# Kernel tuning notes

Measured on AMD Instinct MI355X. Metric: run time of the kernel, lower is better.

The kernel has to match this reference:

```python
import jax, jax.numpy as jnp
import numpy as np

N_NODES = 10000
N_EDGES = 160000
F_IN = 128
H = 8          # heads (both layers)
C1 = 64        # conv1 per-head channels
C2 = 64        # conv2 per-head channels (= out_channels)
NEG_SLOPE = 0.2
EPS = 1e-16


def setup_inputs() -> dict:
    key = jax.random.key(0)
    ks = jax.random.split(key, 12)
    x = jax.random.normal(ks[0], (N_NODES, F_IN), dtype=jnp.float32)
    edge_index = jax.random.randint(ks[1], (2, N_EDGES), 0, N_NODES, dtype=jnp.int32)
    s = lambda fan: float(1.0 / np.sqrt(fan))
    # conv1 params
    W1 = jax.random.normal(ks[2], (F_IN, H * C1), dtype=jnp.float32) * s(F_IN)
    att_src1 = jax.random.normal(ks[3], (H, C1), dtype=jnp.float32) * s(C1)
    att_dst1 = jax.random.normal(ks[4], (H, C1), dtype=jnp.float32) * s(C1)
    bias1 = jnp.zeros((H * C1,), dtype=jnp.float32)
    t1 = jnp.ones((), dtype=jnp.float32)  # SoftmaxAggregation learnable temperature
    # conv2 params (input = H*C1 = 512)
    W2 = jax.random.normal(ks[5], (H * C1, H * C2), dtype=jnp.float32) * s(H * C1)
    att_src2 = jax.random.normal(ks[6], (H, C2), dtype=jnp.float32) * s(C2)
    att_dst2 = jax.random.normal(ks[7], (H, C2), dtype=jnp.float32) * s(C2)
    bias2 = jnp.zeros((H * C2,), dtype=jnp.float32)
    t2 = jnp.ones((), dtype=jnp.float32)
    return {"x": x, "edge_index": edge_index,
            "W1": W1, "att_src1": att_src1, "att_dst1": att_dst1, "bias1": bias1, "t1": t1,
            "W2": W2, "att_src2": att_src2, "att_dst2": att_dst2, "bias2": bias2, "t2": t2}


def _seg_softmax_weights(logits, seg, n):
    # numerically stable softmax over segments (per trailing dims)
    mx = jax.ops.segment_max(logits, seg, num_segments=n)
    mx = jnp.where(jnp.isfinite(mx), mx, 0.0)  # empty segments -> 0
    ex = jnp.exp(logits - mx[seg])
    den = jax.ops.segment_sum(ex, seg, num_segments=n)
    return ex / (den[seg] + EPS)


def gat_layer(x, src, dst, W, a_src, a_dst, bias, t, n):
    # GATConv (add_self_loops=False, concat=True) with SoftmaxAggregation(learn=True)
    h = (x @ W).reshape(n, *a_src.shape)                      # [N,H,C]
    alpha_s = jnp.sum(h * a_src, axis=-1)                     # [N,H]
    alpha_d = jnp.sum(h * a_dst, axis=-1)                     # [N,H]
    e = jax.nn.leaky_relu(alpha_s[src] + alpha_d[dst], NEG_SLOPE)  # [E,H]
    alpha = _seg_softmax_weights(e, dst, n)                   # attention softmax per dst
    m = h[src] * alpha[:, :, None]                            # [E,H,C] messages
    w = _seg_softmax_weights(t * m, dst, n)                   # learnable softmax aggregation
    out = jax.ops.segment_sum(w * m, dst, num_segments=n)     # [N,H,C]
    return out.reshape(n, -1) + bias


def reference(x, edge_index, W1, att_src1, att_dst1, bias1, t1,
              W2, att_src2, att_dst2, bias2, t2):
    src, dst = edge_index[0], edge_index[1]
    n = x.shape[0]
    h = jax.nn.relu(gat_layer(x, src, dst, W1, att_src1, att_dst1, bias1, t1, n))
    return jax.nn.relu(gat_layer(h, src, dst, W2, att_src2, att_dst2, bias2, t2, n))
```

## Files before the change

### kernel.cpp

```cpp
#include <hip/hip_runtime.h>
#include <hip/hip_bf16.h>

#define NN 10000
#define NE 160000
#define NH 8
#define NC 64
#define NF 512
#define NEG_SLOPE 0.2f
#define SEPS 1e-16f
#define L2E 1.44269504f

typedef __attribute__((ext_vector_type(8))) short s8v;
typedef __attribute__((ext_vector_type(4))) float f4v;

__device__ __forceinline__ float lrelu(float x) { return x > 0.f ? x : NEG_SLOPE * x; }

__device__ __forceinline__ unsigned short bf16_rn(float f) {
  unsigned int u = __float_as_uint(f);
  return (unsigned short)((u + 0x7FFFu + ((u >> 16) & 1u)) >> 16);
}
__device__ __forceinline__ float bf16_to_f32(unsigned short h) {
  return __uint_as_float(((unsigned int)h) << 16);
}

__global__ void zero_kernel(int* __restrict__ p, int n) {
  int i = blockIdx.x * blockDim.x + threadIdx.x;
  if (i < n) p[i] = 0;
}

__global__ void hist_kernel(const int* __restrict__ dst, int* __restrict__ counts) {
  int e = blockIdx.x * blockDim.x + threadIdx.x;
  if (e < NE) atomicAdd(&counts[dst[e]], 1);
}

__global__ __launch_bounds__(1024) void scan_fast(const int* __restrict__ counts,
                                                  int* __restrict__ row_ptr) {
  __shared__ int part[1024];
  const int tid = threadIdx.x;
  const int base = tid * 16;
  int loc[16];
  int s = 0;
#pragma unroll
  for (int i = 0; i < 16; ++i) {
    int idx = base + i;
    int v = (idx < NN) ? counts[idx] : 0;
    loc[i] = s;
    s += v;
  }
  part[tid] = s;
  __syncthreads();
  for (int off = 1; off < 1024; off <<= 1) {
    int t = (tid >= off) ? part[tid - off] : 0;
    __syncthreads();
    part[tid] += t;
    __syncthreads();
  }
  int pre = (tid > 0) ? part[tid - 1] : 0;
#pragma unroll
  for (int i = 0; i < 16; ++i) {
    int idx = base + i;
    if (idx < NN) row_ptr[idx] = pre + loc[i];
  }
  if (tid == 1023) row_ptr[NN] = part[1023];
}

__global__ void scatter_kernel(const int* __restrict__ dst, const int* __restrict__ row_ptr,
                               int* __restrict__ cursor, int* __restrict__ sorted) {
  int e = blockIdx.x * blockDim.x + threadIdx.x;
  if (e < NE) {
    int d = dst[e];
    int r = atomicAdd(&cursor[d], 1);
    sorted[row_ptr[d] + r] = e;
  }
}

__global__ void split_kernel(const float* __restrict__ in, unsigned short* __restrict__ hi,
                             unsigned short* __restrict__ lo, int n4) {
  int i = blockIdx.x * blockDim.x + threadIdx.x;
  if (i < n4) {
    float4 v = ((const float4*)in)[i];
    float a[4] = {v.x, v.y, v.z, v.w};
    ushort4 h, l;
    unsigned short* hp = (unsigned short*)&h;
    unsigned short* lp = (unsigned short*)&l;
#pragma unroll
    for (int q = 0; q < 4; ++q) {
      unsigned short hb = bf16_rn(a[q]);
      hp[q] = hb;
      lp[q] = bf16_rn(a[q] - bf16_to_f32(hb));
    }
    ((ushort4*)hi)[i] = h;
    ((ushort4*)lo)[i] = l;
  }
}

__global__ __launch_bounds__(256) void tsplit_kernel(const float* __restrict__ W,
                                                     unsigned short* __restrict__ th,
                                                     unsigned short* __restrict__ tl,
                                                     int K, int N) {
  __shared__ float t[32][33];
  const int bx = blockIdx.x * 32;
  const int by = blockIdx.y * 32;
  const int lx = threadIdx.x & 31, ly = threadIdx.x >> 5;
#pragma unroll
  for (int r = 0; r < 32; r += 8)
    t[ly + r][lx] = W[(size_t)(by + ly + r) * N + bx + lx];
  __syncthreads();
#pragma unroll
  for (int r = 0; r < 32; r += 8) {
    float v = t[lx][ly + r];
    unsigned short hb = bf16_rn(v);
    size_t o = (size_t)(bx + ly + r) * K + by + lx;
    th[o] = hb;
    tl[o] = bf16_rn(v - bf16_to_f32(hb));
  }
}

#define GBM 128
#define GBN 64
#define GBK 32

__global__ __launch_bounds__(256) void gemm_bf16(const unsigned short* __restrict__ Ahi,
                                                 const unsigned short* __restrict__ Alo,
                                                 const unsigned short* __restrict__ BThi,
                                                 const unsigned short* __restrict__ BTlo,
                                                 float* __restrict__ C,
                                                 int M, int K, int N) {
  __shared__ s8v smem[1536];
  const int tid = threadIdx.x;
  const int m0 = blockIdx.y * GBM, n0 = blockIdx.x * GBN;
  const int wid = tid >> 6, lane = tid & 63;
  const int wm = wid >> 1, wn = wid & 1;
  const int lr = lane & 15, lb = lane >> 4;

  f4v acc[4][2];
  const f4v fzero = {0.f, 0.f, 0.f, 0.f};
#pragma unroll
  for (int m = 0; m < 4; ++m)
#pragma unroll
    for (int n = 0; n < 2; ++n) acc[m][n] = fzero;

  const int arow = tid >> 1, akh = tid & 1;
  const bool avalid = (m0 + arow) < M;
  const int aslot = ((arow >> 4) * 4 + akh * 2) * 16 + (arow & 15);
  const int bcol = tid >> 2, bkq = tid & 3;
  const int bslot = ((bcol >> 4) * 4 + bkq) * 16 + (bcol & 15);
  const s8v zv = {0, 0, 0, 0, 0, 0, 0, 0};

  for (int k0 = 0; k0 < K; k0 += GBK) {
    s8v a_h0 = zv, a_h1 = zv, a_l0 = zv, a_l1 = zv, b_h, b_l;
    if (avalid) {
      const unsigned short* ap = &Ahi[(size_t)(m0 + arow) * K + k0 + akh * 16];
      const unsigned short* alp = &Alo[(size_t)(m0 + arow) * K + k0 + akh * 16];
      a_h0 = *(const s8v*)ap;
      a_h1 = *(const s8v*)(ap + 8);
      a_l0 = *(const s8v*)alp;
      a_l1 = *(const s8v*)(alp + 8);
    }
    {
      const unsigned short* bp = &BThi[(size_t)(n0 + bcol) * K + k0 + bkq * 8];
      const unsigned short* blp = &BTlo[(size_t)(n0 + bcol) * K + k0 + bkq * 8];
      b_h = *(const s8v*)bp;
      b_l = *(const s8v*)blp;
    }
    __syncthreads();
    smem[aslot] = a_h0;
    smem[aslot + 16] = a_h1;
    smem[512 + aslot] = a_l0;
    smem[512 + aslot + 16] = a_l1;
    smem[1024 + bslot] = b_h;
    smem[1280 + bslot] = b_l;
    __syncthreads();
    s8v ah[4], al[4], bh[2], bl[2];
#pragma unroll
    for (int m = 0; m < 4; ++m) {
      int slot = ((wm * 4 + m) * 4 + lb) * 16 + lr;
      ah[m] = smem[slot];
      al[m] = smem[512 + slot];
    }
#pragma unroll
    for (int n = 0; n < 2; ++n) {
      int slot = ((wn * 2 + n) * 4 + lb) * 16 + lr;
      bh[n] = smem[1024 + slot];
      bl[n] = smem[1280 + slot];
    }
#pragma unroll
    for (int m = 0; m < 4; ++m)
#pragma unroll
      for (int n = 0; n < 2; ++n) {
        acc[m][n] = __builtin_amdgcn_mfma_f32_16x16x32_bf16(ah[m], bh[n], acc[m][n], 0, 0, 0);
        acc[m][n] = __builtin_amdgcn_mfma_f32_16x16x32_bf16(ah[m], bl[n], acc[m][n], 0, 0, 0);
        acc[m][n] = __builtin_amdgcn_mfma_f32_16x16x32_bf16(al[m], bh[n], acc[m][n], 0, 0, 0);
      }
  }
#pragma unroll
  for (int m = 0; m < 4; ++m) {
    int row = m0 + wm * 64 + m * 16 + lb * 4;
#pragma unroll
    for (int n = 0; n < 2; ++n) {
      int col = n0 + wn * 32 + n * 16 + lr;
#pragma unroll
      for (int j = 0; j < 4; ++j) {
        if (row + j < M) C[(size_t)(row + j) * N + col] = acc[m][n][j];
      }
    }
  }
}

__global__ __launch_bounds__(64) void att_logits_v(const float* __restrict__ h,
                                                   const float* __restrict__ att_src,
                                                   const float* __restrict__ att_dst,
                                                   float* __restrict__ as_,
                                                   float* __restrict__ ad_) {
  const int n = blockIdx.x;
  const int lane = threadIdx.x;
  const float4* hp = (const float4*)&h[(size_t)n * NF];
  float4 v0 = hp[lane * 2], v1 = hp[lane * 2 + 1];
  const int base = lane * 8;
  const float4* sp = (const float4*)&att_src[base];
  const float4* dp = (const float4*)&att_dst[base];
  float4 s0 = sp[0], s1 = sp[1], d0 = dp[0], d1 = dp[1];
  float s = v0.x * s0.x + v0.y * s0.y + v0.z * s0.z + v0.w * s0.w +
            v1.x * s1.x + v1.y * s1.y + v1.z * s1.z + v1.w * s1.w;
  float d = v0.x * d0.x + v0.y * d0.y + v0.z * d0.z + v0.w * d0.w +
            v1.x * d1.x + v1.y * d1.y + v1.z * d1.z + v1.w * d1.w;
#pragma unroll
  for (int off = 1; off <= 4; off <<= 1) {
    s += __shfl_xor(s, off);
    d += __shfl_xor(d, off);
  }
  if ((lane & 7) == 0) {
    int hd = lane >> 3;
    as_[n * NH + hd] = s;
    ad_[n * NH + hd] = d;
  }
}

__global__ __launch_bounds__(256) void agg_fused(const float* __restrict__ h,
                                                 const float* __restrict__ tptr,
                                                 const int* __restrict__ src,
                                                 const int* __restrict__ sorted,
                                                 const int* __restrict__ row_ptr,
                                                 const float* __restrict__ as_,
                                                 const float* __restrict__ ad_,
                                                 const float* __restrict__ bias,
                                                 float* __restrict__ out) {
  __shared__ int s_src[256];
  __shared__ float s_x[256 * NH];
  __shared__ float s_ad[NH], s_inv[NH];
  const int n = blockIdx.x;
  const int tid = threadIdx.x;
  const int hd = tid >> 5;
  const int l32 = tid & 31;
  const int start = row_ptr[n];
  const int deg = row_ptr[n + 1] - start;
  const int c = tid * 2;
  const float tl2 = tptr[0] * L2E;

  if (tid < NH) s_ad[tid] = ad_[n * NH + tid];
  __syncthreads();

  const bool cacheable = (deg <= 256);
  float denh = 0.f;
  for (int base = 0; base < deg; base += 256) {
    int cnt = min(deg - base, 256);
    if (tid < cnt) s_src[tid] = src[sorted[start + base + tid]];
    __syncthreads();
    float adn = s_ad[hd];
    for (int j = l32; j < cnt; j += 32) {
      float e = __builtin_exp2f(L2E * lrelu(as_[s_src[j] * NH + hd] + adn));
      if (cacheable) s_x[j * NH + hd] = e;
      denh += e;
    }
    __syncthreads();
  }
#pragma unroll
  for (int off = 16; off > 0; off >>= 1) denh += __shfl_xor(denh, off);
  if (l32 == 0) s_inv[hd] = 1.f / (denh + SEPS);
  __syncthreads();

  float S0 = 0.f, S1 = 0.f, O0 = 0.f, O1 = 0.f;
  if (cacheable) {
    for (int idx = tid; idx < deg * NH; idx += 256) s_x[idx] *= s_inv[idx & 7];
    __syncthreads();
#pragma unroll 4
    for (int k = 0; k < deg; ++k) {
      int sn = s_src[k];
      float a = s_x[k * NH + hd];
      float2 hv = *(const float2*)&h[(size_t)sn * NF + c];
      float m0 = hv.x * a, m1 = hv.y * a;
      float e0 = __builtin_exp2f(tl2 * m0);
      float e1 = __builtin_exp2f(tl2 * m1);
      S0 += e0; O0 += e0 * m0;
      S1 += e1; O1 += e1 * m1;
    }
  } else {
    for (int base = 0; base < deg; base += 256) {
      int cnt = min(deg - base, 256);
      __syncthreads();
      if (tid < cnt) s_src[tid] = src[sorted[start + base + tid]];
      __syncthreads();
      for (int j = l32; j < cnt; j += 32)
        s_x[j * NH + hd] =
            __builtin_exp2f(L2E * lrelu(as_[s_src[j] * NH + hd] + s_ad[hd])) * s_inv[hd];
      __syncthreads();
      for (int k = 0; k < cnt; ++k) {
        int sn = s_src[k];
        float a = s_x[k * NH + hd];
        float2 hv = *(const float2*)&h[(size_t)sn * NF + c];
        float m0 = hv.x * a, m1 = hv.y * a;
        float e0 = __builtin_exp2f(tl2 * m0);
        float e1 = __builtin_exp2f(tl2 * m1);
        S0 += e0; O0 += e0 * m0;
        S1 += e1; O1 += e1 * m1;
      }
    }
  }
  float r0 = O0 / (S0 + SEPS) + bias[c];
  float r1 = O1 / (S1 + SEPS) + bias[c + 1];
  *(float2*)&out[(size_t)n * NF + c] = make_float2(fmaxf(r0, 0.f), fmaxf(r1, 0.f));
}

extern "C" void kernel_launch(void* const* d_in, const int* in_sizes, int n_in,
                              void* d_out, int out_size, void* d_ws, size_t ws_size,
                              hipStream_t stream) {
  const float* x     = (const float*)d_in[0];
  const int*   ei    = (const int*)d_in[1];
  const float* W1    = (const float*)d_in[2];
  const float* at_s1 = (const float*)d_in[3];
  const float* at_d1 = (const float*)d_in[4];
  const float* b1    = (const float*)d_in[5];
  const float* t1    = (const float*)d_in[6];
  const float* W2    = (const float*)d_in[7];
  const float* at_s2 = (const float*)d_in[8];
  const float* at_d2 = (const float*)d_in[9];
  const float* b2    = (const float*)d_in[10];
  const float* t2    = (const float*)d_in[11];
  float* out = (float*)d_out;

  const int* srcp = ei;
  const int* dstp = ei + NE;

  float* ws = (float*)d_ws;
  float* h_buf = ws;
  float* o_buf = h_buf + (size_t)NN * NF;
  float* asb   = o_buf + (size_t)NN * NF;
  float* adb   = asb + NN * NH;
  unsigned short* xs_hi = (unsigned short*)(adb + NN * NH);
  unsigned short* xs_lo = xs_hi + (size_t)NN * 128;
  unsigned short* wt1h  = xs_lo + (size_t)NN * 128;
  unsigned short* wt1l  = wt1h + 512 * 128;
  unsigned short* wt2h  = wt1l + 512 * 128;
  unsigned short* wt2l  = wt2h + 512 * 512;
  int* counts  = (int*)(wt2l + 512 * 512);
  int* row_ptr = counts + NN;
  int* cursor  = row_ptr + NN + 1;
  int* sorted  = cursor + NN;
  unsigned short* y1h = (unsigned short*)h_buf;
  unsigned short* y1l = y1h + (size_t)NN * NF;

  zero_kernel<<<(NN + 255) / 256, 256, 0, stream>>>(counts, NN);
  zero_kernel<<<(NN + 255) / 256, 256, 0, stream>>>(cursor, NN);
  hist_kernel<<<(NE + 255) / 256, 256, 0, stream>>>(dstp, counts);
  scan_fast<<<1, 1024, 0, stream>>>(counts, row_ptr);
  scatter_kernel<<<(NE + 255) / 256, 256, 0, stream>>>(dstp, row_ptr, cursor, sorted);

  split_kernel<<<(NN * 128 / 4 + 255) / 256, 256, 0, stream>>>(x, xs_hi, xs_lo, NN * 128 / 4);
  tsplit_kernel<<<dim3(512 / 32, 128 / 32), 256, 0, stream>>>(W1, wt1h, wt1l, 128, 512);
  tsplit_kernel<<<dim3(512 / 32, 512 / 32), 256, 0, stream>>>(W2, wt2h, wt2l, 512, 512);

  dim3 ggrid(NF / GBN, (NN + GBM - 1) / GBM);

  gemm_bf16<<<ggrid, 256, 0, stream>>>(xs_hi, xs_lo, wt1h, wt1l, h_buf, NN, 128, NF);
  att_logits_v<<<NN, 64, 0, stream>>>(h_buf, at_s1, at_d1, asb, adb);
  agg_fused<<<NN, 256, 0, stream>>>(h_buf, t1, srcp, sorted, row_ptr, asb, adb, b1, o_buf);

  split_kernel<<<((size_t)NN * NF / 4 + 255) / 256, 256, 0, stream>>>(o_buf, y1h, y1l,
                                                                      NN * NF / 4);
  gemm_bf16<<<ggrid, 256, 0, stream>>>(y1h, y1l, wt2h, wt2l, o_buf, NN, NF, NF);
  att_logits_v<<<NN, 64, 0, stream>>>(o_buf, at_s2, at_d2, asb, adb);
  agg_fused<<<NN, 256, 0, stream>>>(o_buf, t2, srcp, sorted, row_ptr, asb, adb, b2, out);
}
```

Measured before the change: 289.7 us.

## Rewrite aggregation as one-wave kernel, fuse bf16 split, direct-load GEMM

The aggregation kernel becomes a single 64-lane wave per node with 8 channels per lane, using shuffles instead of shared memory and barriers. Attention weights are recomputed on the fly rather than cached. Layer 1's output is written directly as bf16 hi/lo pairs, which removes a separate split pass and an fp32 round trip. The GEMM drops shared-memory staging in favour of direct global loads with a larger 128x128 tile. The CSR now stores source ids directly, and memsets replace the zero kernels. The cost is fewer threads per node for gather latency hiding, and GEMM operand reuse that depends on the cache instead of LDS.

```diff
diff --git a/kernel.cpp b/kernel.cpp
--- a/kernel.cpp
+++ b/kernel.cpp
@@ -23,11 +23,6 @@
   return __uint_as_float(((unsigned int)h) << 16);
 }
 
-__global__ void zero_kernel(int* __restrict__ p, int n) {
-  int i = blockIdx.x * blockDim.x + threadIdx.x;
-  if (i < n) p[i] = 0;
-}
-
 __global__ void hist_kernel(const int* __restrict__ dst, int* __restrict__ counts) {
   int e = blockIdx.x * blockDim.x + threadIdx.x;
   if (e < NE) atomicAdd(&counts[dst[e]], 1);
@@ -64,13 +59,14 @@
   if (tid == 1023) row_ptr[NN] = part[1023];
 }
 
-__global__ void scatter_kernel(const int* __restrict__ dst, const int* __restrict__ row_ptr,
-                               int* __restrict__ cursor, int* __restrict__ sorted) {
+__global__ void scatter_src(const int* __restrict__ src, const int* __restrict__ dst,
+                            const int* __restrict__ row_ptr, int* __restrict__ cursor,
+                            int* __restrict__ csr_src) {
   int e = blockIdx.x * blockDim.x + threadIdx.x;
   if (e < NE) {
     int d = dst[e];
     int r = atomicAdd(&cursor[d], 1);
-    sorted[row_ptr[d] + r] = e;
+    csr_src[row_ptr[d] + r] = src[e];
   }
 }
 
@@ -116,78 +112,62 @@
   }
 }
 
-#define GBM 128
-#define GBN 64
-#define GBK 32
-
-__global__ __launch_bounds__(256) void gemm_bf16(const unsigned short* __restrict__ Ahi,
-                                                 const unsigned short* __restrict__ Alo,
-                                                 const unsigned short* __restrict__ BThi,
-                                                 const unsigned short* __restrict__ BTlo,
-                                                 float* __restrict__ C,
-                                                 int M, int K, int N) {
-  __shared__ s8v smem[1536];
+__global__ __launch_bounds__(256) void gemm_dg(const unsigned short* __restrict__ Ahi,
+                                               const unsigned short* __restrict__ Alo,
+                                               const unsigned short* __restrict__ BThi,
+                                               const unsigned short* __restrict__ BTlo,
+                                               float* __restrict__ C,
+                                               int M, int K, int N) {
   const int tid = threadIdx.x;
-  const int m0 = blockIdx.y * GBM, n0 = blockIdx.x * GBN;
   const int wid = tid >> 6, lane = tid & 63;
   const int wm = wid >> 1, wn = wid & 1;
   const int lr = lane & 15, lb = lane >> 4;
-
-  f4v acc[4][2];
+  const int m0 = blockIdx.y * 128 + wm * 64;
+  const int n0 = blockIdx.x * 128 + wn * 64;
+
+  f4v acc[4][4];
   const f4v fzero = {0.f, 0.f, 0.f, 0.f};
 #pragma unroll
   for (int m = 0; m < 4; ++m)
 #pragma unroll
-    for (int n = 0; n < 2; ++n) acc[m][n] = fzero;
-
-  const int arow = tid >> 1, akh = tid & 1;
-  const bool avalid = (m0 + arow) < M;
-  const int aslot = ((arow >> 4) * 4 + akh * 2) * 16 + (arow & 15);
-  const int bcol = tid >> 2, bkq = tid & 3;
-  const int bslot = ((bcol >> 4) * 4 + bkq) * 16 + (bcol & 15);
-  const s8v zv = {0, 0, 0, 0, 0, 0, 0, 0};
-
-  for (int k0 = 0; k0 < K; k0 += GBK) {
-    s8v a_h0 = zv, a_h1 = zv, a_l0 = zv, a_l1 = zv, b_h, b_l;
-    if (avalid) {
-      const unsigned short* ap = &Ahi[(size_t)(m0 + arow) * K + k0 + akh * 16];
-      const unsigned short* alp = &Alo[(size_t)(m0 + arow) * K + k0 + akh * 16];
-      a_h0 = *(const s8v*)ap;
-      a_h1 = *(const s8v*)(ap + 8);
-      a_l0 = *(const s8v*)alp;
-      a_l1 = *(const s8v*)(alp + 8);
-    }
-    {
-      const unsigned short* bp = &BThi[(size_t)(n0 + bcol) * K + k0 + bkq * 8];
-      const unsigned short* blp = &BTlo[(size_t)(n0 + bcol) * K + k0 + bkq * 8];
-      b_h = *(const s8v*)bp;
-      b_l = *(const s8v*)blp;
-    }
-    __syncthreads();
-    smem[aslot] = a_h0;
-    smem[aslot + 16] = a_h1;
-    smem[512 + aslot] = a_l0;
-    smem[512 + aslot + 16] = a_l1;
-    smem[1024 + bslot] = b_h;
-    smem[1280 + bslot] = b_l;
-    __syncthreads();
-    s8v ah[4], al[4], bh[2], bl[2];
+    for (int n = 0; n < 4; ++n) acc[m][n] = fzero;
+
+  const unsigned short* aph[4];
+  const unsigned short* apl[4];
+  const unsigned short* bph[4];
+  const unsigned short* bpl[4];
+#pragma unroll
+  for (int m = 0; m < 4; ++m) {
+    int row = m0 + m * 16 + lr;
+    row = row < M ? row : M - 1;
+    size_t o = (size_t)row * K + lb * 8;
+    aph[m] = Ahi + o;
+    apl[m] = Alo + o;
+  }
+#pragma unroll
+  for (int n = 0; n < 4; ++n) {
+    int col = n0 + n * 16 + lr;
+    size_t o = (size_t)col * K + lb * 8;
+    bph[n] = BThi + o;
+    bpl[n] = BTlo + o;
+  }
+
+  for (int k0 = 0; k0 < K; k0 += 32) {
+    s8v ah[4], al[4], bh[4], bl[4];
 #pragma unroll
     for (int m = 0; m < 4; ++m) {
-      int slot = ((wm * 4 + m) * 4 + lb) * 16 + lr;
-      ah[m] = smem[slot];
-      al[m] = smem[512 + slot];
-    }
-#pragma unroll
-    for (int n = 0; n < 2; ++n) {
-      int slot = ((wn * 2 + n) * 4 + lb) * 16 + lr;
-      bh[n] = smem[1024 + slot];
-      bl[n] = smem[1280 + slot];
+      ah[m] = *(const s8v*)(aph[m] + k0);
+      al[m] = *(const s8v*)(apl[m] + k0);
+    }
+#pragma unroll
+    for (int n = 0; n < 4; ++n) {
+      bh[n] = *(const s8v*)(bph[n] + k0);
+      bl[n] = *(const s8v*)(bpl[n] + k0);
     }
 #pragma unroll
     for (int m = 0; m < 4; ++m)
 #pragma unroll
-      for (int n = 0; n < 2; ++n) {
+      for (int n = 0; n < 4; ++n) {
         acc[m][n] = __builtin_amdgcn_mfma_f32_16x16x32_bf16(ah[m], bh[n], acc[m][n], 0, 0, 0);
         acc[m][n] = __builtin_amdgcn_mfma_f32_16x16x32_bf16(ah[m], bl[n], acc[m][n], 0, 0, 0);
         acc[m][n] = __builtin_amdgcn_mfma_f32_16x16x32_bf16(al[m], bh[n], acc[m][n], 0, 0, 0);
@@ -195,13 +175,13 @@
   }
 #pragma unroll
   for (int m = 0; m < 4; ++m) {
-    int row = m0 + wm * 64 + m * 16 + lb * 4;
-#pragma unroll
-    for (int n = 0; n < 2; ++n) {
-      int col = n0 + wn * 32 + n * 16 + lr;
+    int rowb = m0 + m * 16 + lb * 4;
+#pragma unroll
+    for (int n = 0; n < 4; ++n) {
+      int col = n0 + n * 16 + lr;
 #pragma unroll
       for (int j = 0; j < 4; ++j) {
-        if (row + j < M) C[(size_t)(row + j) * N + col] = acc[m][n][j];
+        if (rowb + j < M) C[(size_t)(rowb + j) * N + col] = acc[m][n][j];
       }
     }
   }
@@ -236,89 +216,90 @@
   }
 }
 
-__global__ __launch_bounds__(256) void agg_fused(const float* __restrict__ h,
-                                                 const float* __restrict__ tptr,
-                                                 const int* __restrict__ src,
-                                                 const int* __restrict__ sorted,
-                                                 const int* __restrict__ row_ptr,
-                                                 const float* __restrict__ as_,
-                                                 const float* __restrict__ ad_,
-                                                 const float* __restrict__ bias,
-                                                 float* __restrict__ out) {
-  __shared__ int s_src[256];
-  __shared__ float s_x[256 * NH];
-  __shared__ float s_ad[NH], s_inv[NH];
+template <int SPLITOUT>
+__global__ __launch_bounds__(64) void agg64(const float* __restrict__ h,
+                                            const float* __restrict__ tptr,
+                                            const int* __restrict__ csr_src,
+                                            const int* __restrict__ row_ptr,
+                                            const float* __restrict__ as_,
+                                            const float* __restrict__ ad_,
+                                            const float* __restrict__ bias,
+                                            float* __restrict__ outf,
+                                            unsigned short* __restrict__ outh,
+                                            unsigned short* __restrict__ outl) {
   const int n = blockIdx.x;
-  const int tid = threadIdx.x;
-  const int hd = tid >> 5;
-  const int l32 = tid & 31;
+  const int lane = threadIdx.x;
   const int start = row_ptr[n];
   const int deg = row_ptr[n + 1] - start;
-  const int c = tid * 2;
+  const int hd1 = lane & 7;
+  const int jof = lane >> 3;
+  const int hd2 = lane >> 3;
+  const int c = lane * 8;
   const float tl2 = tptr[0] * L2E;
-
-  if (tid < NH) s_ad[tid] = ad_[n * NH + tid];
-  __syncthreads();
-
-  const bool cacheable = (deg <= 256);
-  float denh = 0.f;
-  for (int base = 0; base < deg; base += 256) {
-    int cnt = min(deg - base, 256);
-    if (tid < cnt) s_src[tid] = src[sorted[start + base + tid]];
-    __syncthreads();
-    float adn = s_ad[hd];
-    for (int j = l32; j < cnt; j += 32) {
-      float e = __builtin_exp2f(L2E * lrelu(as_[s_src[j] * NH + hd] + adn));
-      if (cacheable) s_x[j * NH + hd] = e;
-      denh += e;
-    }
-    __syncthreads();
-  }
-#pragma unroll
-  for (int off = 16; off > 0; off >>= 1) denh += __shfl_xor(denh, off);
-  if (l32 == 0) s_inv[hd] = 1.f / (denh + SEPS);
-  __syncthreads();
-
-  float S0 = 0.f, S1 = 0.f, O0 = 0.f, O1 = 0.f;
-  if (cacheable) {
-    for (int idx = tid; idx < deg * NH; idx += 256) s_x[idx] *= s_inv[idx & 7];
-    __syncthreads();
-#pragma unroll 4
-    for (int k = 0; k < deg; ++k) {
-      int sn = s_src[k];
-      float a = s_x[k * NH + hd];
-      float2 hv = *(const float2*)&h[(size_t)sn * NF + c];
-      float m0 = hv.x * a, m1 = hv.y * a;
-      float e0 = __builtin_exp2f(tl2 * m0);
-      float e1 = __builtin_exp2f(tl2 * m1);
-      S0 += e0; O0 += e0 * m0;
-      S1 += e1; O1 += e1 * m1;
-    }
+  const float adv = ad_[n * NH + hd1];
+
+  float den = 0.f;
+  for (int base = 0; base < deg; base += 64) {
+    int cnt = min(deg - base, 64);
+    int mysrc = csr_src[start + base + min(lane, cnt - 1)];
+    int trips = (cnt + 7) >> 3;
+    for (int i = 0; i < trips; ++i) {
+      int j = jof + (i << 3);
+      int sn = __shfl(mysrc, min(j, cnt - 1));
+      float v = __builtin_exp2f(L2E * lrelu(as_[sn * NH + hd1] + adv));
+      den += (j < cnt) ? v : 0.f;
+    }
+  }
+  den += __shfl_xor(den, 8);
+  den += __shfl_xor(den, 16);
+  den += __shfl_xor(den, 32);
+  float invd = 1.f / (den + SEPS);
+  float inv2 = __shfl(invd, hd2);
+  float adv2 = __shfl(adv, hd2);
+
+  float S[8], O[8];
+#pragma unroll
+  for (int q = 0; q < 8; ++q) { S[q] = 0.f; O[q] = 0.f; }
+  for (int base = 0; base < deg; base += 64) {
+    int cnt = min(deg - base, 64);
+    int mysrc = csr_src[start + base + min(lane, cnt - 1)];
+    for (int k = 0; k < cnt; ++k) {
+      int sn = __shfl(mysrc, k);
+      float av = as_[sn * NH + hd2];
+      float alpha = __builtin_exp2f(L2E * lrelu(av + adv2)) * inv2;
+      const float* hp = &h[(size_t)sn * NF + c];
+      float4 h0 = *(const float4*)hp;
+      float4 h1 = *(const float4*)(hp + 4);
+      float hv[8] = {h0.x, h0.y, h0.z, h0.w, h1.x, h1.y, h1.z, h1.w};
+#pragma unroll
+      for (int q = 0; q < 8; ++q) {
+        float m = hv[q] * alpha;
+        float e = __builtin_exp2f(tl2 * m);
+        S[q] += e;
+        O[q] = fmaf(e, m, O[q]);
+      }
+    }
+  }
+  float r[8];
+#pragma unroll
+  for (int q = 0; q < 8; ++q)
+    r[q] = fmaxf(O[q] / (S[q] + SEPS) + bias[c + q], 0.f);
+
+  if (SPLITOUT) {
+    short hh[8], ll[8];
+#pragma unroll
+    for (int q = 0; q < 8; ++q) {
+      unsigned short hb = bf16_rn(r[q]);
+      hh[q] = (short)hb;
+      ll[q] = (short)bf16_rn(r[q] - bf16_to_f32(hb));
+    }
+    *(s8v*)(outh + (size_t)n * NF + c) = s8v{hh[0], hh[1], hh[2], hh[3], hh[4], hh[5], hh[6], hh[7]};
+    *(s8v*)(outl + (size_t)n * NF + c) = s8v{ll[0], ll[1], ll[2], ll[3], ll[4], ll[5], ll[6], ll[7]};
   } else {
-    for (int base = 0; base < deg; base += 256) {
-      int cnt = min(deg - base, 256);
-      __syncthreads();
-      if (tid < cnt) s_src[tid] = src[sorted[start + base + tid]];
-      __syncthreads();
-      for (int j = l32; j < cnt; j += 32)
-        s_x[j * NH + hd] =
-            __builtin_exp2f(L2E * lrelu(as_[s_src[j] * NH + hd] + s_ad[hd])) * s_inv[hd];
-      __syncthreads();
-      for (int k = 0; k < cnt; ++k) {
-        int sn = s_src[k];
-        float a = s_x[k * NH + hd];
-        float2 hv = *(const float2*)&h[(size_t)sn * NF + c];
-        float m0 = hv.x * a, m1 = hv.y * a;
-        float e0 = __builtin_exp2f(tl2 * m0);
-        float e1 = __builtin_exp2f(tl2 * m1);
-        S0 += e0; O0 += e0 * m0;
-        S1 += e1; O1 += e1 * m1;
-      }
-    }
-  }
-  float r0 = O0 / (S0 + SEPS) + bias[c];
-  float r1 = O1 / (S1 + SEPS) + bias[c + 1];
-  *(float2*)&out[(size_t)n * NF + c] = make_float2(fmaxf(r0, 0.f), fmaxf(r1, 0.f));
+    float* op = &outf[(size_t)n * NF + c];
+    *(float4*)op = make_float4(r[0], r[1], r[2], r[3]);
+    *(float4*)(op + 4) = make_float4(r[4], r[5], r[6], r[7]);
+  }
 }
 
 extern "C" void kernel_launch(void* const* d_in, const int* in_sizes, int n_in,
@@ -343,8 +324,7 @@
 
   float* ws = (float*)d_ws;
   float* h_buf = ws;
-  float* o_buf = h_buf + (size_t)NN * NF;
-  float* asb   = o_buf + (size_t)NN * NF;
+  float* asb   = h_buf + (size_t)NN * NF;
   float* adb   = asb + NN * NH;
   unsigned short* xs_hi = (unsigned short*)(adb + NN * NH);
   unsigned short* xs_lo = xs_hi + (size_t)NN * 128;
@@ -352,32 +332,32 @@
   unsigned short* wt1l  = wt1h + 512 * 128;
   unsigned short* wt2h  = wt1l + 512 * 128;
   unsigned short* wt2l  = wt2h + 512 * 512;
-  int* counts  = (int*)(wt2l + 512 * 512);
+  unsigned short* y1h   = wt2l + 512 * 512;
+  unsigned short* y1l   = y1h + (size_t)NN * NF;
+  int* counts  = (int*)(y1l + (size_t)NN * NF);
   int* row_ptr = counts + NN;
   int* cursor  = row_ptr + NN + 1;
-  int* sorted  = cursor + NN;
-  unsigned short* y1h = (unsigned short*)h_buf;
-  unsigned short* y1l = y1h + (size_t)NN * NF;
-
-  zero_kernel<<<(NN + 255) / 256, 256, 0, stream>>>(counts, NN);
-  zero_kernel<<<(NN + 255) / 256, 256, 0, stream>>>(cursor, NN);
+  int* csr_src = cursor + NN;
+
+  hipMemsetAsync(counts, 0, NN * sizeof(int), stream);
+  hipMemsetAsync(cursor, 0, NN * sizeof(int), stream);
   hist_kernel<<<(NE + 255) / 256, 256, 0, stream>>>(dstp, counts);
   scan_fast<<<1, 1024, 0, stream>>>(counts, row_ptr);
-  scatter_kernel<<<(NE + 255) / 256, 256, 0, stream>>>(dstp, row_ptr, cursor, sorted);
+  scatter_src<<<(NE + 255) / 256, 256, 0, stream>>>(srcp, dstp, row_ptr, cursor, csr_src);
 
   split_kernel<<<(NN * 128 / 4 + 255) / 256, 256, 0, stream>>>(x, xs_hi, xs_lo, NN * 128 / 4);
   tsplit_kernel<<<dim3(512 / 32, 128 / 32), 256, 0, stream>>>(W1, wt1h, wt1l, 128, 512);
   tsplit_kernel<<<dim3(512 / 32, 512 / 32), 256, 0, stream>>>(W2, wt2h, wt2l, 512, 512);
 
-  dim3 ggrid(NF / GBN, (NN + GBM - 1) / GBM);
-
-  gemm_bf16<<<ggrid, 256, 0, stream>>>(xs_hi, xs_lo, wt1h, wt1l, h_buf, NN, 128, NF);
+  dim3 ggrid(NF / 128, (NN + 127) / 128);
+
+  gemm_dg<<<ggrid, 256, 0, stream>>>(xs_hi, xs_lo, wt1h, wt1l, h_buf, NN, 128, NF);
   att_logits_v<<<NN, 64, 0, stream>>>(h_buf, at_s1, at_d1, asb, adb);
-  agg_fused<<<NN, 256, 0, stream>>>(h_buf, t1, srcp, sorted, row_ptr, asb, adb, b1, o_buf);
-
-  split_kernel<<<((size_t)NN * NF / 4 + 255) / 256, 256, 0, stream>>>(o_buf, y1h, y1l,
-                                                                      NN * NF / 4);
-  gemm_bf16<<<ggrid, 256, 0, stream>>>(y1h, y1l, wt2h, wt2l, o_buf, NN, NF, NF);
-  att_logits_v<<<NN, 64, 0, stream>>>(o_buf, at_s2, at_d2, asb, adb);
-  agg_fused<<<NN, 256, 0, stream>>>(o_buf, t2, srcp, sorted, row_ptr, asb, adb, b2, out);
-}
+  agg64<1><<<NN, 64, 0, stream>>>(h_buf, t1, csr_src, row_ptr, asb, adb, b1,
+                                  nullptr, y1h, y1l);
+
+  gemm_dg<<<ggrid, 256, 0, stream>>>(y1h, y1l, wt2h, wt2l, h_buf, NN, NF, NF);
+  att_logits_v<<<NN, 64, 0, stream>>>(h_buf, at_s2, at_d2, asb, adb);
+  agg64<0><<<NN, 64, 0, stream>>>(h_buf, t2, csr_src, row_ptr, asb, adb, b2,
+                                  out, nullptr, nullptr);
+}
```

New measurement: 326.4 us. 12.7% more time.
